# Optimization experiments

Measured on AMD Instinct MI355X. Metric: run time of the kernel, lower is better.

Reference implementation:

```python
import jax, jax.numpy as jnp
import numpy as np

NUM_NODES = 200000
NUM_EDGES = 500000
B = 4096            # batch size (src, dst, neg each B)
ND = 3 * B          # dst nodes of attention block
K = 10              # sampled neighbors per dst
N = ND * (1 + K)    # total tail nodes
D = 128             # dim_embed == dim_node
DE = 128            # dim_edge
DT = 128            # dim_time
H = 2               # num_heads
DIN = 2 * D + DE + DT  # GRUCell input dim


def time_encode(t, w, b):
    # tglite TimeEncode: cos(t * w + b)
    return jnp.cos(t[..., None] * w + b)


def gru_cell(x, h, w_ih, w_hh, b_ih, b_hh):
    # torch.nn.GRUCell, gate order [r, z, n]
    gi = x @ w_ih.T + b_ih
    gh = h @ w_hh.T + b_hh
    i_r, i_z, i_n = jnp.split(gi, 3, axis=-1)
    h_r, h_z, h_n = jnp.split(gh, 3, axis=-1)
    r = jax.nn.sigmoid(i_r + h_r)
    z = jax.nn.sigmoid(i_z + h_z)
    n = jnp.tanh(i_n + r * h_n)
    return (1.0 - z) * n + z * h


def setup_inputs() -> dict:
    key = jax.random.key(0)
    ks = jax.random.split(key, 40)
    p = lambda i, shape: jax.random.normal(ks[i], shape, dtype=jnp.float32) * 0.05
    return {
        "nodes": jax.random.randint(ks[0], (N,), 0, NUM_NODES),
        "eids": jax.random.randint(ks[1], (ND, K), 0, NUM_EDGES),
        "dt_nbr": jax.random.uniform(ks[2], (ND, K), dtype=jnp.float32) * 1000.0,
        "nfeat": p(3, (NUM_NODES, D)),
        "mem_data": p(4, (NUM_NODES, D)),
        "mem_time": jax.random.uniform(ks[5], (NUM_NODES,), dtype=jnp.float32) * 1000.0,
        "mail_data": p(6, (NUM_NODES, 2 * D + DE)),
        "mail_time": jax.random.uniform(ks[7], (NUM_NODES,), dtype=jnp.float32) * 1000.0,
        "efeat": p(8, (NUM_EDGES, DE)),
        "time_w": p(9, (DT,)),
        "time_b": p(10, (DT,)),
        "gru_w_ih": p(11, (3 * D, DIN)),
        "gru_w_hh": p(12, (3 * D, D)),
        "gru_b_ih": p(13, (3 * D,)),
        "gru_b_hh": p(14, (3 * D,)),
        "wq": p(15, (D, D + DT)), "bq": p(16, (D,)),
        "wk": p(17, (D, D + DE + DT)), "bk": p(18, (D,)),
        "wv": p(19, (D, D + DE + DT)), "bv": p(20, (D,)),
        "wo": p(21, (D, 2 * D)), "bo": p(22, (D,)),
        "ln_g": jnp.ones((D,), jnp.float32), "ln_b": jnp.zeros((D,), jnp.float32),
        "ep_sw": p(23, (D, D)), "ep_sb": p(24, (D,)),
        "ep_dw": p(25, (D, D)), "ep_db": p(26, (D,)),
        "ep_ow": p(27, (1, D)), "ep_ob": p(28, (1,)),
    }


def reference(nodes, eids, dt_nbr, nfeat, mem_data, mem_time, mail_data, mail_time,
              efeat, time_w, time_b, gru_w_ih, gru_w_hh, gru_b_ih, gru_b_hh,
              wq, bq, wk, bk, wv, bv, wo, bo, ln_g, ln_b,
              ep_sw, ep_sb, ep_dw, ep_db, ep_ow, ep_ob):
    # ---- update_memory: gather mailbox/memory, time-encode delta, GRUCell ----
    delta = mail_time[nodes] - mem_time[nodes]                  # [N]
    tenc = time_encode(delta, time_w, time_b)                   # [N, DT]
    mail = jnp.concatenate([mail_data[nodes], tenc], axis=1)    # [N, DIN]
    mem = gru_cell(mail, mem_data[nodes], gru_w_ih, gru_w_hh, gru_b_ih, gru_b_hh)  # [N, D]
    # (blk.g.mem.update(nodes, mem, mail_ts) is a persistent-state side effect)

    h = nfeat[nodes] + mem                                      # dst/src hidden states
    dst_h = h[:ND]                                              # [ND, D]
    src_h = h[ND:].reshape(ND, K, D)                            # [ND, K, D]

    # ---- TemporalAttnLayer (TGL-style multi-head attention over neighbors) ----
    zero_tenc = jnp.broadcast_to(jnp.cos(time_b), (ND, DT))     # time_encode(0)
    Q = jnp.concatenate([dst_h, zero_tenc], axis=1) @ wq.T + bq # [ND, D]
    tenc_n = time_encode(dt_nbr, time_w, time_b)                # [ND, K, DT]
    k_in = jnp.concatenate([src_h, efeat[eids], tenc_n], axis=-1)  # [ND, K, D+DE+DT]
    Kf = k_in @ wk.T + bk                                       # [ND, K, D]
    Vf = k_in @ wv.T + bv                                       # [ND, K, D]

    dh = D // H
    Qh = Q.reshape(ND, H, dh)
    Kh = Kf.reshape(ND, K, H, dh)
    Vh = Vf.reshape(ND, K, H, dh)
    att = jax.nn.softmax(jnp.einsum('nhd,nkhd->nkh', Qh, Kh), axis=1)  # [ND, K, H]
    agg = jnp.einsum('nkh,nkhd->nhd', att, Vh).reshape(ND, D)   # [ND, D]

    out = jnp.concatenate([dst_h, agg], axis=1) @ wo.T + bo     # [ND, D]
    out = jax.nn.relu(out)
    mu = out.mean(axis=-1, keepdims=True)
    var = out.var(axis=-1, keepdims=True)
    emb = ln_g * (out - mu) * jax.lax.rsqrt(var + 1e-5) + ln_b  # LayerNorm

    # ---- EdgePredictor over (src, dst) and (src, neg) splits ----
    src_e, dst_e, neg_e = emb[:B], emb[B:2 * B], emb[2 * B:]
    s_proj = src_e @ ep_sw.T + ep_sb
    pos = jax.nn.relu(s_proj + dst_e @ ep_dw.T + ep_db) @ ep_ow.T + ep_ob  # [B, 1]
    neg = jax.nn.relu(s_proj + neg_e @ ep_dw.T + ep_db) @ ep_ow.T + ep_ob  # [B, 1]
    return jnp.concatenate([pos, neg], axis=1)                  # [B, 2]
```

## Files before the change

kernel.cpp:

```cpp
#include <hip/hip_runtime.h>

constexpr int ND_   = 12288;
constexpr int K_    = 10;
constexpr int NTOT  = ND_ * (1 + K_);
constexpr int B_    = 4096;
constexpr int RKV   = ND_ * K_;

constexpr size_t OFF_QB   = 0;
constexpr size_t OFF_AGG  = 786432;
constexpr size_t OFF_HB   = 43253760;
constexpr size_t OFF_KVB  = 51904512;
constexpr size_t OFF_EMB  = 67633152;
constexpr size_t OFF_WCAT = 69206016;
constexpr size_t OFF_WKV  = 69369856;
constexpr size_t OFF_BCAT = 69419008;
constexpr size_t OFF_BKV  = 69419520;
constexpr size_t OFF_WQB  = 69419776;
constexpr size_t OFF_WOB  = 69427968;
constexpr size_t OFF_SWP  = 69444352;
constexpr size_t OFF_DWP  = 69460736;
constexpr size_t OFF_QZ   = 69477120;

#define DEVFN __device__ __forceinline__

typedef __attribute__((ext_vector_type(8))) short bf16x8;
typedef __attribute__((ext_vector_type(4))) float f32x4;
#define MFMA16(a, b, c) __builtin_amdgcn_mfma_f32_16x16x32_bf16((a), (b), (c), 0, 0, 0)

DEVFN unsigned short f2bf(float x) {
  unsigned int u = __float_as_uint(x);
  u = (u + 0x7FFFu + ((u >> 16) & 1u)) >> 16;
  return (unsigned short)u;
}
DEVFN float bf2f(unsigned short h) { return __uint_as_float(((unsigned int)h) << 16); }

DEVFN bf16x8 packcvt(float4 a, float4 b) {
  union { unsigned int u[4]; bf16x8 v; } r;
  asm("v_cvt_pk_bf16_f32 %0, %1, %2" : "=v"(r.u[0]) : "v"(a.x), "v"(a.y));
  asm("v_cvt_pk_bf16_f32 %0, %1, %2" : "=v"(r.u[1]) : "v"(a.z), "v"(a.w));
  asm("v_cvt_pk_bf16_f32 %0, %1, %2" : "=v"(r.u[2]) : "v"(b.x), "v"(b.y));
  asm("v_cvt_pk_bf16_f32 %0, %1, %2" : "=v"(r.u[3]) : "v"(b.z), "v"(b.w));
  return r.v;
}

DEVFN float dot4(const float4 a, const float4 b, float acc) {
  acc = fmaf(a.x, b.x, acc);
  acc = fmaf(a.y, b.y, acc);
  acc = fmaf(a.z, b.z, acc);
  acc = fmaf(a.w, b.w, acc);
  return acc;
}
DEVFN float sigmoidf_(float x) { return 1.0f / (1.0f + expf(-x)); }

__global__ void k0_all(const float* __restrict__ w_ih, const float* __restrict__ w_hh,
                       const float* __restrict__ wk,   const float* __restrict__ wv,
                       const float* __restrict__ wq,   const float* __restrict__ wo,
                       const float* __restrict__ sw,   const float* __restrict__ dwm,
                       const float* __restrict__ b_ih, const float* __restrict__ b_hh,
                       const float* __restrict__ bk,   const float* __restrict__ bv,
                       const float* __restrict__ time_b, const float* __restrict__ bq,
                       unsigned short* __restrict__ WcatP, unsigned short* __restrict__ WkvP,
                       unsigned short* __restrict__ WqB,   unsigned short* __restrict__ WoB,
                       float4* __restrict__ SwP, float4* __restrict__ DwP,
                       float* __restrict__ bcat, float* __restrict__ bkv,
                       float* __restrict__ qzero)
{
  int gid = blockIdx.x * 256 + threadIdx.x;
  if (gid < 327680) {
    int f = gid >> 9, idx = gid & 511;
    int l = idx >> 3, j8 = idx & 7;
    int kt = f >> 5, nt = f & 31;
    int k = kt * 32 + (l >> 4) * 8 + j8;
    int c = nt * 16 + (l & 15);
    int q = c >> 7, jb = (c >> 6) & 1, g = (c >> 4) & 3, j = q * 32 + jb * 16 + (c & 15);
    float w;
    if (g == 0)      w = (k < 512) ? w_ih[(size_t)j * 512 + k]         : w_hh[(size_t)j * 128 + (k - 512)];
    else if (g == 1) w = (k < 512) ? w_ih[(size_t)(128 + j) * 512 + k] : w_hh[(size_t)(128 + j) * 128 + (k - 512)];
    else if (g == 2) w = (k < 512) ? w_ih[(size_t)(256 + j) * 512 + k] : 0.0f;
    else             w = (k < 512) ? 0.0f : w_hh[(size_t)(256 + j) * 128 + (k - 512)];
    WcatP[gid] = f2bf(w);
    return;
  }
  gid -= 327680;
  if (gid < 98304) {
    int f = gid >> 9, idx = gid & 511;
    int l = idx >> 3, j8 = idx & 7;
    int kt = f >> 4, nt = f & 15;
    int k = kt * 32 + (l >> 4) * 8 + j8;
    int c = nt * 16 + (l & 15);
    float w = (c < 128) ? wk[(size_t)c * 384 + k] : wv[(size_t)(c - 128) * 384 + k];
    WkvP[gid] = f2bf(w);
    return;
  }
  gid -= 98304;
  if (gid < 49152) {
    if (gid < 16384) {
      int f = gid >> 9, idx = gid & 511;
      int l = idx >> 3, j8 = idx & 7;
      int kt = f >> 3, nt = f & 7;
      int k = kt * 32 + (l >> 4) * 8 + j8;
      int c = nt * 16 + (l & 15);
      WqB[gid] = f2bf(wq[(size_t)c * 256 + k]);
    } else {
      int g2 = gid - 16384;
      int f = g2 >> 9, idx = g2 & 511;
      int l = idx >> 3, j8 = idx & 7;
      int kt = f >> 3, nt = f & 7;
      int k = kt * 32 + (l >> 4) * 8 + j8;
      int c = nt * 16 + (l & 15);
      WoB[g2] = f2bf(wo[(size_t)c * 256 + k]);
    }
    return;
  }
  gid -= 49152;
  if (gid < 8960) {
    if (gid < 4096) {
      int k4 = gid / 128, c = gid % 128;
      const float* s = sw + c * 128 + 4 * k4;
      SwP[gid] = make_float4(s[0], s[1], s[2], s[3]);
    } else if (gid < 8192) {
      int id = gid - 4096;
      int k4 = id / 128, c = id % 128;
      const float* s = dwm + c * 128 + 4 * k4;
      DwP[id] = make_float4(s[0], s[1], s[2], s[3]);
    } else if (gid < 8704) {
      int id = gid - 8192;
      int q = id >> 7, jb = (id >> 6) & 1, g = (id >> 4) & 3, lcc = id & 15;
      int j = q * 32 + jb * 16 + lcc;
      float b;
      if (g == 0)      b = b_ih[j] + b_hh[j];
      else if (g == 1) b = b_ih[128 + j] + b_hh[128 + j];
      else if (g == 2) b = b_ih[256 + j];
      else             b = b_hh[256 + j];
      bcat[id] = b;
    } else {
      int id = gid - 8704;
      bkv[id] = (id < 128) ? bk[id] : bv[id - 128];
    }
    return;
  }
  gid -= 8960;
  if (gid < 128) {
    float acc = bq[gid];
    for (int k = 0; k < 128; ++k)
      acc = fmaf(cosf(time_b[k]), wq[gid * 256 + 128 + k], acc);
    qzero[gid] = acc;
  }
}

__global__ __launch_bounds__(512) void k1_fused(
    const int* __restrict__ nodes, const float* __restrict__ mail_data,
    const float* __restrict__ mem_data, const float* __restrict__ mail_time,
    const float* __restrict__ mem_time, const float* __restrict__ time_w,
    const float* __restrict__ time_b, const unsigned short* __restrict__ WcatP,
    const float* __restrict__ bcat, const float* __restrict__ nfeat,
    unsigned short* __restrict__ hb)
{
  __shared__ unsigned short As[20 * 1024];
  __shared__ int nid[32];
  __shared__ float dd[32];
  const int tid = threadIdx.x;
  const int rbase = blockIdx.x * 32;
  if (tid < 32) {
    int n = nodes[rbase + tid];
    nid[tid] = n;
    dd[tid] = mail_time[n] - mem_time[n];
  }
  __syncthreads();

  {
    const int sr = tid & 31, tcol = tid >> 5;
    const int sc4 = tcol & 7, koff = tcol >> 3;
    const int n = nid[sr];
    const float drow = dd[sr];
    const float* mailp = mail_data + (size_t)n * 384;
    const float* memp  = mem_data  + (size_t)n * 128;
    const int half = sr >> 4, r15 = sr & 15, q = sc4 >> 1;
    const int slot = half * 64 + q * 16 + ((r15 + 4 * q) & 15);
    char* wbase = (char*)As + slot * 16 + (sc4 & 1) * 8;
    #pragma unroll
    for (int i = 0; i < 10; ++i) {
      const int kt = 2 * i + koff;
      const int c0 = kt * 32 + sc4 * 4;
      float4 v;
      if (i < 6) {
        v = *(const float4*)(mailp + c0);
      } else if (i >= 8) {
        v = *(const float4*)(memp + c0 - 512);
      } else {
        const float4 w0 = *(const float4*)(time_w + (c0 - 384));
        const float4 b0 = *(const float4*)(time_b + (c0 - 384));
        v.x = cosf(fmaf(drow, w0.x, b0.x)); v.y = cosf(fmaf(drow, w0.y, b0.y));
        v.z = cosf(fmaf(drow, w0.z, b0.z)); v.w = cosf(fmaf(drow, w0.w, b0.w));
      }
      unsigned int pk0, pk1;
      asm("v_cvt_pk_bf16_f32 %0, %1, %2" : "=v"(pk0) : "v"(v.x), "v"(v.y));
      asm("v_cvt_pk_bf16_f32 %0, %1, %2" : "=v"(pk1) : "v"(v.z), "v"(v.w));
      *(uint2*)(wbase + kt * 2048) = make_uint2(pk0, pk1);
    }
  }
  __syncthreads();

  const int w = tid >> 6, l = tid & 63;
  const int lr = l >> 4, lc = l & 15;
  const unsigned short* Bp = WcatP + (size_t)(w * 4) * 512 + l * 8;
  const int slotA = lr * 16 + ((lc + 4 * lr) & 15);
  const char* rbA = (const char*)As + slotA * 16;

  f32x4 acc[2][4];
  #pragma unroll
  for (int m = 0; m < 2; ++m)
    #pragma unroll
    for (int bn = 0; bn < 4; ++bn) acc[m][bn] = (f32x4){0.f, 0.f, 0.f, 0.f};

  #pragma unroll
  for (int kt = 0; kt < 20; ++kt) {
    const bf16x8 A0 = *(const bf16x8*)(rbA + kt * 2048);
    const bf16x8 A1 = *(const bf16x8*)(rbA + kt * 2048 + 1024);
    #pragma unroll
    for (int bn = 0; bn < 4; ++bn) {
      const bf16x8 Bf = *(const bf16x8*)(Bp + ((size_t)kt * 32 + bn) * 512);
      acc[0][bn] = MFMA16(A0, Bf, acc[0][bn]);
      acc[1][bn] = MFMA16(A1, Bf, acc[1][bn]);
    }
  }

  const int jcol = (w >> 1) * 32 + (w & 1) * 16 + lc;
  float bg[4];
  #pragma unroll
  for (int g = 0; g < 4; ++g) bg[g] = bcat[w * 64 + g * 16 + lc];

  #pragma unroll
  for (int mt = 0; mt < 2; ++mt) {
    #pragma unroll
    for (int rr = 0; rr < 4; ++rr) {
      const int rloc = mt * 16 + lr * 4 + rr;
      const int grow = rbase + rloc;
      const int n2   = nid[rloc];
      const float aR  = acc[mt][0][rr] + bg[0];
      const float aZ  = acc[mt][1][rr] + bg[1];
      const float aNi = acc[mt][2][rr] + bg[2];
      const float aNh = acc[mt][3][rr] + bg[3];
      const float r_  = sigmoidf_(aR);
      const float z_  = sigmoidf_(aZ);
      const float n_  = tanhf(aNi + r_ * aNh);
      const float mem = mem_data[(size_t)n2 * 128 + jcol];
      const float h = nfeat[(size_t)n2 * 128 + jcol] + (1.0f - z_) * n_ + z_ * mem;
      hb[(size_t)grow * 128 + jcol] = f2bf(h);
    }
  }
}

DEVFN void k2s(const unsigned short* __restrict__ WkvP, int kt, int wn, int l,
               bf16x8 a, f32x4 (&acc)[4]) {
  #pragma unroll
  for (int bn = 0; bn < 4; ++bn) {
    const bf16x8 b = *(const bf16x8*)(WkvP + ((size_t)(kt * 16 + wn * 4 + bn) * 64 + l) * 8);
    acc[bn] = MFMA16(a, b, acc[bn]);
  }
}

__global__ __launch_bounds__(512) void k2_fused(
    const unsigned short* __restrict__ hb, const int* __restrict__ eids,
    const float* __restrict__ dt_nbr, const float* __restrict__ efeat,
    const float* __restrict__ time_w, const float* __restrict__ time_b,
    const unsigned short* __restrict__ WkvP, const float* __restrict__ bkv,
    unsigned short* __restrict__ KVb)
{
  const int w = threadIdx.x >> 6, l = threadIdx.x & 63;
  const int wm = w >> 2, wn = w & 3;
  const int lr = l >> 4, lc = l & 15;
  const int t16 = blockIdx.x * 2 + wm;
  const int rbase = t16 * 16;

  int eld = 0; float dld = 0.f;
  if (l < 16) { eld = eids[rbase + l]; dld = dt_nbr[rbase + l]; }
  const int   eid = __shfl(eld, lc);
  const float dt  = __shfl(dld, lc);

  const float* ep = efeat + (size_t)eid * 128 + lr * 8;
  bf16x8 ea[4];
  #pragma unroll
  for (int qq = 0; qq < 4; ++qq)
    ea[qq] = packcvt(((const float4*)(ep + qq * 32))[0], ((const float4*)(ep + qq * 32))[1]);
  const unsigned short* hp = hb + (size_t)(ND_ + rbase + lc) * 128 + lr * 8;
  bf16x8 hh[4];
  #pragma unroll
  for (int qq = 0; qq < 4; ++qq) hh[qq] = *(const bf16x8*)(hp + qq * 32);
  bf16x8 tt[4];
  #pragma unroll
  for (int qq = 0; qq < 4; ++qq) {
    const int c0 = qq * 32 + lr * 8;
    const float4 w0 = ((const float4*)(time_w + c0))[0];
    const float4 w1 = ((const float4*)(time_w + c0))[1];
    const float4 b0 = ((const float4*)(time_b + c0))[0];
    const float4 b1 = ((const float4*)(time_b + c0))[1];
    float4 u, v;
    u.x = cosf(fmaf(dt, w0.x, b0.x)); u.y = cosf(fmaf(dt, w0.y, b0.y));
    u.z = cosf(fmaf(dt, w0.z, b0.z)); u.w = cosf(fmaf(dt, w0.w, b0.w));
    v.x = cosf(fmaf(dt, w1.x, b1.x)); v.y = cosf(fmaf(dt, w1.y, b1.y));
    v.z = cosf(fmaf(dt, w1.z, b1.z)); v.w = cosf(fmaf(dt, w1.w, b1.w));
    tt[qq] = packcvt(u, v);
  }

  f32x4 acc[4];
  #pragma unroll
  for (int bn = 0; bn < 4; ++bn) acc[bn] = (f32x4){0.f, 0.f, 0.f, 0.f};

  #pragma unroll
  for (int qq = 0; qq < 4; ++qq) k2s(WkvP, qq, wn, l, hh[qq], acc);
  #pragma unroll
  for (int qq = 0; qq < 4; ++qq) k2s(WkvP, 4 + qq, wn, l, ea[qq], acc);
  #pragma unroll
  for (int qq = 0; qq < 4; ++qq) k2s(WkvP, 8 + qq, wn, l, tt[qq], acc);

  float bb[4];
  #pragma unroll
  for (int bn = 0; bn < 4; ++bn) bb[bn] = bkv[wn * 64 + bn * 16 + lc];

  #pragma unroll
  for (int rr = 0; rr < 4; ++rr) {
    const size_t grow = (size_t)(rbase + lr * 4 + rr);
    #pragma unroll
    for (int bn = 0; bn < 4; ++bn)
      KVb[grow * 256 + wn * 64 + bn * 16 + lc] = f2bf(acc[bn][rr] + bb[bn]);
  }
}

__global__ __launch_bounds__(512) void kQ_gemm(
    const unsigned short* __restrict__ hb, const unsigned short* __restrict__ WqB,
    const float* __restrict__ qzero, unsigned short* __restrict__ Qb)
{
  const int w = threadIdx.x >> 6, l = threadIdx.x & 63;
  const int wm = w >> 2, wn = w & 3;
  const int lr = l >> 4, lc = l & 15;
  const int t16base = blockIdx.x * 4 + wm * 2;
  const unsigned short* Ar0 = hb + (size_t)(t16base * 16 + lc) * 128 + lr * 8;
  const unsigned short* Ar1 = Ar0 + 16 * 128;

  f32x4 acc[2][2];
  #pragma unroll
  for (int m = 0; m < 2; ++m)
    #pragma unroll
    for (int bn = 0; bn < 2; ++bn) acc[m][bn] = (f32x4){0.f, 0.f, 0.f, 0.f};

  #pragma unroll
  for (int kt = 0; kt < 4; ++kt) {
    const bf16x8 a0 = *(const bf16x8*)(Ar0 + kt * 32);
    const bf16x8 a1 = *(const bf16x8*)(Ar1 + kt * 32);
    #pragma unroll
    for (int bn = 0; bn < 2; ++bn) {
      const bf16x8 b = *(const bf16x8*)(WqB + ((size_t)(kt * 8 + wn * 2 + bn) * 64 + l) * 8);
      acc[0][bn] = MFMA16(a0, b, acc[0][bn]);
      acc[1][bn] = MFMA16(a1, b, acc[1][bn]);
    }
  }

  #pragma unroll
  for (int mt = 0; mt < 2; ++mt)
    #pragma unroll
    for (int rr = 0; rr < 4; ++rr) {
      const int row = (t16base + mt) * 16 + lr * 4 + rr;
      #pragma unroll
      for (int bn = 0; bn < 2; ++bn) {
        const int col = (wn * 2 + bn) * 16 + lc;
        Qb[(size_t)row * 128 + col] = f2bf(acc[mt][bn][rr] + qzero[col]);
      }
    }
}

__global__ __launch_bounds__(256) void kAtt(
    const unsigned short* __restrict__ Qb, const unsigned short* __restrict__ KVb,
    unsigned short* __restrict__ aggb)
{
  const int w = threadIdx.x >> 6, l = threadIdx.x & 63;
  const int i = blockIdx.x * 4 + w;
  const float q0 = bf2f(Qb[(size_t)i * 128 + l]);
  const float q1 = bf2f(Qb[(size_t)i * 128 + 64 + l]);
  const unsigned short* base = KVb + (size_t)i * K_ * 256;

  float s0[K_], s1[K_], v0[K_], v1[K_];
  #pragma unroll
  for (int kk = 0; kk < K_; ++kk) {
    const unsigned short* rp = base + kk * 256;
    const float k0 = bf2f(rp[l]);
    const float k1 = bf2f(rp[64 + l]);
    v0[kk] = bf2f(rp[128 + l]);
    v1[kk] = bf2f(rp[192 + l]);
    float p0 = q0 * k0, p1 = q1 * k1;
    #pragma unroll
    for (int t = 32; t; t >>= 1) { p0 += __shfl_xor(p0, t); p1 += __shfl_xor(p1, t); }
    s0[kk] = p0; s1[kk] = p1;
  }
  float m0 = s0[0], m1 = s1[0];
  #pragma unroll
  for (int kk = 1; kk < K_; ++kk) { m0 = fmaxf(m0, s0[kk]); m1 = fmaxf(m1, s1[kk]); }
  float sum0 = 0.f, sum1 = 0.f, a0 = 0.f, a1 = 0.f;
  #pragma unroll
  for (int kk = 0; kk < K_; ++kk) {
    const float e0 = expf(s0[kk] - m0);
    const float e1 = expf(s1[kk] - m1);
    sum0 += e0; sum1 += e1;
    a0 += e0 * v0[kk]; a1 += e1 * v1[kk];
  }
  aggb[(size_t)i * 128 + l]      = f2bf(a0 / sum0);
  aggb[(size_t)i * 128 + 64 + l] = f2bf(a1 / sum1);
}

__global__ __launch_bounds__(512) void kO_ln(
    const unsigned short* __restrict__ hb, const unsigned short* __restrict__ aggb,
    const unsigned short* __restrict__ WoB, const float* __restrict__ bo,
    const float* __restrict__ ln_g, const float* __restrict__ ln_b,
    float* __restrict__ emb)
{
  __shared__ float ps[64][4], pq[64][4];
  const int w = threadIdx.x >> 6, l = threadIdx.x & 63;
  const int wm = w >> 2, wn = w & 3;
  const int lr = l >> 4, lc = l & 15;
  const int t16base = blockIdx.x * 4 + wm * 2;
  const unsigned short* Ah0 = hb   + (size_t)(t16base * 16 + lc) * 128 + lr * 8;
  const unsigned short* Ah1 = Ah0 + 16 * 128;
  const unsigned short* Ag0 = aggb + (size_t)(t16base * 16 + lc) * 128 + lr * 8;
  const unsigned short* Ag1 = Ag0 + 16 * 128;

  f32x4 acc[2][2];
  #pragma unroll
  for (int m = 0; m < 2; ++m)
    #pragma unroll
    for (int bn = 0; bn < 2; ++bn) acc[m][bn] = (f32x4){0.f, 0.f, 0.f, 0.f};

  #pragma unroll
  for (int kt = 0; kt < 8; ++kt) {
    const bf16x8 a0 = (kt < 4) ? *(const bf16x8*)(Ah0 + kt * 32)
                               : *(const bf16x8*)(Ag0 + (kt - 4) * 32);
    const bf16x8 a1 = (kt < 4) ? *(const bf16x8*)(Ah1 + kt * 32)
                               : *(const bf16x8*)(Ag1 + (kt - 4) * 32);
    #pragma unroll
    for (int bn = 0; bn < 2; ++bn) {
      const bf16x8 b = *(const bf16x8*)(WoB + ((size_t)(kt * 8 + wn * 2 + bn) * 64 + l) * 8);
      acc[0][bn] = MFMA16(a0, b, acc[0][bn]);
      acc[1][bn] = MFMA16(a1, b, acc[1][bn]);
    }
  }

  const int c0 = (wn * 2) * 16 + lc, c1 = c0 + 16;
  const float b0v = bo[c0], b1v = bo[c1];
  float xv0[2][4], xv1[2][4];
  #pragma unroll
  for (int mt = 0; mt < 2; ++mt)
    #pragma unroll
    for (int rr = 0; rr < 4; ++rr) {
      const float x0 = fmaxf(acc[mt][0][rr] + b0v, 0.f);
      const float x1 = fmaxf(acc[mt][1][rr] + b1v, 0.f);
      xv0[mt][rr] = x0; xv1[mt][rr] = x1;
      float s = x0 + x1, q = x0 * x0 + x1 * x1;
      #pragma unroll
      for (int t = 8; t; t >>= 1) { s += __shfl_xor(s, t); q += __shfl_xor(q, t); }
      const int rloc = (wm * 2 + mt) * 16 + lr * 4 + rr;
      if (lc == 0) { ps[rloc][wn] = s; pq[rloc][wn] = q; }
    }
  __syncthreads();
  const float g0 = ln_g[c0], g1 = ln_g[c1], lb0 = ln_b[c0], lb1 = ln_b[c1];
  #pragma unroll
  for (int mt = 0; mt < 2; ++mt)
    #pragma unroll
    for (int rr = 0; rr < 4; ++rr) {
      const int rloc = (wm * 2 + mt) * 16 + lr * 4 + rr;
      const int row  = blockIdx.x * 64 + rloc;
      const float sum = ps[rloc][0] + ps[rloc][1] + ps[rloc][2] + ps[rloc][3];
      const float sq  = pq[rloc][0] + pq[rloc][1] + pq[rloc][2] + pq[rloc][3];
      const float mu  = sum * (1.0f / 128.0f);
      const float var = sq * (1.0f / 128.0f) - mu * mu;
      const float rs  = rsqrtf(var + 1e-5f);
      emb[(size_t)row * 128 + c0] = g0 * (xv0[mt][rr] - mu) * rs + lb0;
      emb[(size_t)row * 128 + c1] = g1 * (xv1[mt][rr] - mu) * rs + lb1;
    }
}

__global__ __launch_bounds__(128) void k3_ep(
    const float* __restrict__ emb, const float4* __restrict__ SwP,
    const float4* __restrict__ DwP, const float* __restrict__ ep_sb,
    const float* __restrict__ ep_db, const float* __restrict__ ep_ow,
    const float* __restrict__ ep_ob, float* __restrict__ out)
{
  __shared__ float se[128], de[128], ne[128];
  __shared__ float redp[2], redn[2];
  const int c = threadIdx.x;
  const int i = blockIdx.x;
  se[c] = emb[(size_t)i * 128 + c];
  de[c] = emb[(size_t)(B_ + i) * 128 + c];
  ne[c] = emb[(size_t)(2 * B_ + i) * 128 + c];
  __syncthreads();
  float sacc = ep_sb[c], dacc = ep_db[c], nacc = ep_db[c];
  for (int k4 = 0; k4 < 32; ++k4) {
    const float4 sw = SwP[k4 * 128 + c];
    const float4 dw = DwP[k4 * 128 + c];
    sacc = dot4(((const float4*)se)[k4], sw, sacc);
    dacc = dot4(((const float4*)de)[k4], dw, dacc);
    nacc = dot4(((const float4*)ne)[k4], dw, nacc);
  }
  const float ow = ep_ow[c];
  float pp = fmaxf(sacc + dacc, 0.f) * ow;
  float pn = fmaxf(sacc + nacc, 0.f) * ow;
  for (int t = 32; t; t >>= 1) { pp += __shfl_xor(pp, t); pn += __shfl_xor(pn, t); }
  if ((c & 63) == 0) { redp[c >> 6] = pp; redn[c >> 6] = pn; }
  __syncthreads();
  if (c == 0) {
    const float ob = ep_ob[0];
    out[i * 2]     = redp[0] + redp[1] + ob;
    out[i * 2 + 1] = redn[0] + redn[1] + ob;
  }
}

extern "C" void kernel_launch(void* const* d_in, const int* in_sizes, int n_in,
                              void* d_out, int out_size, void* d_ws, size_t ws_size,
                              hipStream_t stream) {
  const int*   nodes     = (const int*)d_in[0];
  const int*   eids      = (const int*)d_in[1];
  const float* dt_nbr    = (const float*)d_in[2];
  const float* nfeat     = (const float*)d_in[3];
  const float* mem_data  = (const float*)d_in[4];
  const float* mem_time  = (const float*)d_in[5];
  const float* mail_data = (const float*)d_in[6];
  const float* mail_time = (const float*)d_in[7];
  const float* efeat     = (const float*)d_in[8];
  const float* time_w    = (const float*)d_in[9];
  const float* time_b    = (const float*)d_in[10];
  const float* gru_w_ih  = (const float*)d_in[11];
  const float* gru_w_hh  = (const float*)d_in[12];
  const float* gru_b_ih  = (const float*)d_in[13];
  const float* gru_b_hh  = (const float*)d_in[14];
  const float* wq        = (const float*)d_in[15];
  const float* bq        = (const float*)d_in[16];
  const float* wk        = (const float*)d_in[17];
  const float* bk        = (const float*)d_in[18];
  const float* wv        = (const float*)d_in[19];
  const float* bv        = (const float*)d_in[20];
  const float* wo        = (const float*)d_in[21];
  const float* bo        = (const float*)d_in[22];
  const float* ln_g      = (const float*)d_in[23];
  const float* ln_b      = (const float*)d_in[24];
  const float* ep_sw     = (const float*)d_in[25];
  const float* ep_sb     = (const float*)d_in[26];
  const float* ep_dw     = (const float*)d_in[27];
  const float* ep_db     = (const float*)d_in[28];
  const float* ep_ow     = (const float*)d_in[29];
  const float* ep_ob     = (const float*)d_in[30];
  float* out = (float*)d_out;
  float* ws  = (float*)d_ws;

  unsigned short* Qb    = (unsigned short*)(ws + OFF_QB);
  unsigned short* aggb  = (unsigned short*)(ws + OFF_AGG);
  unsigned short* hb    = (unsigned short*)(ws + OFF_HB);
  unsigned short* KVb   = (unsigned short*)(ws + OFF_KVB);
  float*          emb   = ws + OFF_EMB;
  unsigned short* WcatP = (unsigned short*)(ws + OFF_WCAT);
  unsigned short* WkvP  = (unsigned short*)(ws + OFF_WKV);
  float*          bcat  = ws + OFF_BCAT;
  float*          bkv   = ws + OFF_BKV;
  unsigned short* WqB   = (unsigned short*)(ws + OFF_WQB);
  unsigned short* WoB   = (unsigned short*)(ws + OFF_WOB);
  float4*         SwP   = (float4*)(ws + OFF_SWP);
  float4*         DwP   = (float4*)(ws + OFF_DWP);
  float*          qzero = ws + OFF_QZ;

  k0_all<<<1892, 256, 0, stream>>>(gru_w_ih, gru_w_hh, wk, wv, wq, wo, ep_sw, ep_dw,
                                   gru_b_ih, gru_b_hh, bk, bv, time_b, bq,
                                   WcatP, WkvP, WqB, WoB, SwP, DwP, bcat, bkv, qzero);
  k1_fused<<<NTOT / 32, 512, 0, stream>>>(nodes, mail_data, mem_data, mail_time,
                                          mem_time, time_w, time_b, WcatP, bcat,
                                          nfeat, hb);
  k2_fused<<<RKV / 32, 512, 0, stream>>>(hb, eids, dt_nbr, efeat, time_w, time_b,
                                         WkvP, bkv, KVb);
  kQ_gemm<<<ND_ / 64, 512, 0, stream>>>(hb, WqB, qzero, Qb);
  kAtt<<<ND_ / 4, 256, 0, stream>>>(Qb, KVb, aggb);
  kO_ln<<<ND_ / 64, 512, 0, stream>>>(hb, aggb, WoB, bo, ln_g, ln_b, emb);
  k3_ep<<<B_, 128, 0, stream>>>(emb, SwP, DwP, ep_sb, ep_db, ep_ow, ep_ob, out);
}
```

Before: 406.5 us.

## Retile GRU kernel to 64-row blocks and switch to fast intrinsic math

The fused memory-update GRU kernel now processes 64 rows per block instead of 32. Each wave computes a 32x128 output tile, so each weight fragment loaded from global memory is reused across twice as many rows. The shared-memory staging layout and gather are rewritten to match, and the launch bounds ask for higher occupancy. Separately, cosf, expf, tanhf and division in the GRU, time-encoding and attention code are replaced with fast intrinsics (__cosf, __expf, __fdividef, an exp-based tanh). This lowers transcendental cost at some loss of accuracy, for example __cosf on time arguments that can reach about 1000*w.

```diff
diff --git a/kernel.cpp b/kernel.cpp
--- a/kernel.cpp
+++ b/kernel.cpp
@@ -50,7 +50,12 @@
   acc = fmaf(a.w, b.w, acc);
   return acc;
 }
-DEVFN float sigmoidf_(float x) { return 1.0f / (1.0f + expf(-x)); }
+DEVFN float fsig(float x)  { return __fdividef(1.0f, 1.0f + __expf(-x)); }
+DEVFN float ftanh(float x) {
+  x = fminf(fmaxf(x, -15.0f), 15.0f);
+  const float t = __expf(2.0f * x);
+  return __fdividef(t - 1.0f, t + 1.0f);
+}
 
 __global__ void k0_all(const float* __restrict__ w_ih, const float* __restrict__ w_hh,
                        const float* __restrict__ wk,   const float* __restrict__ wv,
@@ -148,7 +153,7 @@
   }
 }
 
-__global__ __launch_bounds__(512) void k1_fused(
+__global__ __launch_bounds__(512, 4) void k1_fused(
     const int* __restrict__ nodes, const float* __restrict__ mail_data,
     const float* __restrict__ mem_data, const float* __restrict__ mail_time,
     const float* __restrict__ mem_time, const float* __restrict__ time_w,
@@ -156,97 +161,93 @@
     const float* __restrict__ bcat, const float* __restrict__ nfeat,
     unsigned short* __restrict__ hb)
 {
-  __shared__ unsigned short As[20 * 1024];
-  __shared__ int nid[32];
-  __shared__ float dd[32];
+  __shared__ unsigned short As[20 * 2048];
   const int tid = threadIdx.x;
-  const int rbase = blockIdx.x * 32;
-  if (tid < 32) {
-    int n = nodes[rbase + tid];
-    nid[tid] = n;
-    dd[tid] = mail_time[n] - mem_time[n];
-  }
-  __syncthreads();
+  const int rbase = blockIdx.x * 64;
 
   {
-    const int sr = tid & 31, tcol = tid >> 5;
-    const int sc4 = tcol & 7, koff = tcol >> 3;
-    const int n = nid[sr];
-    const float drow = dd[sr];
+    const int sr = tid & 63, scol = tid >> 6;
+    const int koff = scol >> 2, q = scol & 3;
+    const int n = nodes[rbase + sr];
+    const float drow = mail_time[n] - mem_time[n];
     const float* mailp = mail_data + (size_t)n * 384;
     const float* memp  = mem_data  + (size_t)n * 128;
-    const int half = sr >> 4, r15 = sr & 15, q = sc4 >> 1;
-    const int slot = half * 64 + q * 16 + ((r15 + 4 * q) & 15);
-    char* wbase = (char*)As + slot * 16 + (sc4 & 1) * 8;
+    unsigned short* wb = As + ((size_t)((sr >> 4) * 64 + q * 16 + (sr & 15))) * 8;
     #pragma unroll
     for (int i = 0; i < 10; ++i) {
       const int kt = 2 * i + koff;
-      const int c0 = kt * 32 + sc4 * 4;
-      float4 v;
-      if (i < 6) {
-        v = *(const float4*)(mailp + c0);
-      } else if (i >= 8) {
-        v = *(const float4*)(memp + c0 - 512);
+      const int c0 = kt * 32 + q * 8;
+      float4 v0, v1;
+      if (c0 < 384) {
+        v0 = *(const float4*)(mailp + c0);
+        v1 = *(const float4*)(mailp + c0 + 4);
+      } else if (c0 >= 512) {
+        v0 = *(const float4*)(memp + c0 - 512);
+        v1 = *(const float4*)(memp + c0 - 508);
       } else {
-        const float4 w0 = *(const float4*)(time_w + (c0 - 384));
-        const float4 b0 = *(const float4*)(time_b + (c0 - 384));
-        v.x = cosf(fmaf(drow, w0.x, b0.x)); v.y = cosf(fmaf(drow, w0.y, b0.y));
-        v.z = cosf(fmaf(drow, w0.z, b0.z)); v.w = cosf(fmaf(drow, w0.w, b0.w));
+        const float4 w0 = *(const float4*)(time_w + c0 - 384);
+        const float4 w1 = *(const float4*)(time_w + c0 - 380);
+        const float4 b0 = *(const float4*)(time_b + c0 - 384);
+        const float4 b1 = *(const float4*)(time_b + c0 - 380);
+        v0.x = __cosf(fmaf(drow, w0.x, b0.x)); v0.y = __cosf(fmaf(drow, w0.y, b0.y));
+        v0.z = __cosf(fmaf(drow, w0.z, b0.z)); v0.w = __cosf(fmaf(drow, w0.w, b0.w));
+        v1.x = __cosf(fmaf(drow, w1.x, b1.x)); v1.y = __cosf(fmaf(drow, w1.y, b1.y));
+        v1.z = __cosf(fmaf(drow, w1.z, b1.z)); v1.w = __cosf(fmaf(drow, w1.w, b1.w));
       }
-      unsigned int pk0, pk1;
-      asm("v_cvt_pk_bf16_f32 %0, %1, %2" : "=v"(pk0) : "v"(v.x), "v"(v.y));
-      asm("v_cvt_pk_bf16_f32 %0, %1, %2" : "=v"(pk1) : "v"(v.z), "v"(v.w));
-      *(uint2*)(wbase + kt * 2048) = make_uint2(pk0, pk1);
+      *(bf16x8*)(wb + (size_t)kt * 2048) = packcvt(v0, v1);
     }
   }
   __syncthreads();
 
   const int w = tid >> 6, l = tid & 63;
+  const int wm = w >> 2, wn = w & 3;
   const int lr = l >> 4, lc = l & 15;
-  const unsigned short* Bp = WcatP + (size_t)(w * 4) * 512 + l * 8;
-  const int slotA = lr * 16 + ((lc + 4 * lr) & 15);
-  const char* rbA = (const char*)As + slotA * 16;
-
-  f32x4 acc[2][4];
+  const unsigned short* Bp = WcatP + (size_t)(wn * 8) * 512 + l * 8;
+  const unsigned short* Ab = As + (size_t)(2 * wm) * 512 + (size_t)l * 8;
+
+  f32x4 acc[2][8];
   #pragma unroll
   for (int m = 0; m < 2; ++m)
     #pragma unroll
-    for (int bn = 0; bn < 4; ++bn) acc[m][bn] = (f32x4){0.f, 0.f, 0.f, 0.f};
+    for (int bn = 0; bn < 8; ++bn) acc[m][bn] = (f32x4){0.f, 0.f, 0.f, 0.f};
 
   #pragma unroll
   for (int kt = 0; kt < 20; ++kt) {
-    const bf16x8 A0 = *(const bf16x8*)(rbA + kt * 2048);
-    const bf16x8 A1 = *(const bf16x8*)(rbA + kt * 2048 + 1024);
-    #pragma unroll
-    for (int bn = 0; bn < 4; ++bn) {
+    const bf16x8 A0 = *(const bf16x8*)(Ab + (size_t)kt * 2048);
+    const bf16x8 A1 = *(const bf16x8*)(Ab + (size_t)kt * 2048 + 512);
+    #pragma unroll
+    for (int bn = 0; bn < 8; ++bn) {
       const bf16x8 Bf = *(const bf16x8*)(Bp + ((size_t)kt * 32 + bn) * 512);
       acc[0][bn] = MFMA16(A0, Bf, acc[0][bn]);
       acc[1][bn] = MFMA16(A1, Bf, acc[1][bn]);
     }
   }
 
-  const int jcol = (w >> 1) * 32 + (w & 1) * 16 + lc;
-  float bg[4];
-  #pragma unroll
-  for (int g = 0; g < 4; ++g) bg[g] = bcat[w * 64 + g * 16 + lc];
+  float bg[8];
+  #pragma unroll
+  for (int bn = 0; bn < 8; ++bn) bg[bn] = bcat[wn * 128 + bn * 16 + lc];
 
   #pragma unroll
   for (int mt = 0; mt < 2; ++mt) {
     #pragma unroll
     for (int rr = 0; rr < 4; ++rr) {
-      const int rloc = mt * 16 + lr * 4 + rr;
+      const int rloc = (2 * wm + mt) * 16 + lr * 4 + rr;
       const int grow = rbase + rloc;
-      const int n2   = nid[rloc];
-      const float aR  = acc[mt][0][rr] + bg[0];
-      const float aZ  = acc[mt][1][rr] + bg[1];
-      const float aNi = acc[mt][2][rr] + bg[2];
-      const float aNh = acc[mt][3][rr] + bg[3];
-      const float r_  = sigmoidf_(aR);
-      const float z_  = sigmoidf_(aZ);
-      const float n_  = tanhf(aNi + r_ * aNh);
-      const float mem = mem_data[(size_t)n2 * 128 + jcol];
-      const float h = nfeat[(size_t)n2 * 128 + jcol] + (1.0f - z_) * n_ + z_ * mem;
-      hb[(size_t)grow * 128 + jcol] = f2bf(h);
+      const int n2   = nodes[grow];
+      #pragma unroll
+      for (int jb = 0; jb < 2; ++jb) {
+        const int jcol = wn * 32 + jb * 16 + lc;
+        const float aR  = acc[mt][jb * 4 + 0][rr] + bg[jb * 4 + 0];
+        const float aZ  = acc[mt][jb * 4 + 1][rr] + bg[jb * 4 + 1];
+        const float aNi = acc[mt][jb * 4 + 2][rr] + bg[jb * 4 + 2];
+        const float aNh = acc[mt][jb * 4 + 3][rr] + bg[jb * 4 + 3];
+        const float r_  = fsig(aR);
+        const float z_  = fsig(aZ);
+        const float n_  = ftanh(aNi + r_ * aNh);
+        const float mem = mem_data[(size_t)n2 * 128 + jcol];
+        const float h = nfeat[(size_t)n2 * 128 + jcol] + (1.0f - z_) * n_ + z_ * mem;
+        hb[(size_t)grow * 128 + jcol] = f2bf(h);
+      }
     }
   }
 }
@@ -296,10 +297,10 @@
     const float4 b0 = ((const float4*)(time_b + c0))[0];
     const float4 b1 = ((const float4*)(time_b + c0))[1];
     float4 u, v;
-    u.x = cosf(fmaf(dt, w0.x, b0.x)); u.y = cosf(fmaf(dt, w0.y, b0.y));
-    u.z = cosf(fmaf(dt, w0.z, b0.z)); u.w = cosf(fmaf(dt, w0.w, b0.w));
-    v.x = cosf(fmaf(dt, w1.x, b1.x)); v.y = cosf(fmaf(dt, w1.y, b1.y));
-    v.z = cosf(fmaf(dt, w1.z, b1.z)); v.w = cosf(fmaf(dt, w1.w, b1.w));
+    u.x = __cosf(fmaf(dt, w0.x, b0.x)); u.y = __cosf(fmaf(dt, w0.y, b0.y));
+    u.z = __cosf(fmaf(dt, w0.z, b0.z)); u.w = __cosf(fmaf(dt, w0.w, b0.w));
+    v.x = __cosf(fmaf(dt, w1.x, b1.x)); v.y = __cosf(fmaf(dt, w1.y, b1.y));
+    v.z = __cosf(fmaf(dt, w1.z, b1.z)); v.w = __cosf(fmaf(dt, w1.w, b1.w));
     tt[qq] = packcvt(u, v);
   }
 
@@ -398,13 +399,13 @@
   float sum0 = 0.f, sum1 = 0.f, a0 = 0.f, a1 = 0.f;
   #pragma unroll
   for (int kk = 0; kk < K_; ++kk) {
-    const float e0 = expf(s0[kk] - m0);
-    const float e1 = expf(s1[kk] - m1);
+    const float e0 = __expf(s0[kk] - m0);
+    const float e1 = __expf(s1[kk] - m1);
     sum0 += e0; sum1 += e1;
     a0 += e0 * v0[kk]; a1 += e1 * v1[kk];
   }
-  aggb[(size_t)i * 128 + l]      = f2bf(a0 / sum0);
-  aggb[(size_t)i * 128 + 64 + l] = f2bf(a1 / sum1);
+  aggb[(size_t)i * 128 + l]      = f2bf(__fdividef(a0, sum0));
+  aggb[(size_t)i * 128 + 64 + l] = f2bf(__fdividef(a1, sum1));
 }
 
 __global__ __launch_bounds__(512) void kO_ln(
@@ -567,7 +568,7 @@
   k0_all<<<1892, 256, 0, stream>>>(gru_w_ih, gru_w_hh, wk, wv, wq, wo, ep_sw, ep_dw,
                                    gru_b_ih, gru_b_hh, bk, bv, time_b, bq,
                                    WcatP, WkvP, WqB, WoB, SwP, DwP, bcat, bkv, qzero);
-  k1_fused<<<NTOT / 32, 512, 0, stream>>>(nodes, mail_data, mem_data, mail_time,
+  k1_fused<<<NTOT / 64, 512, 0, stream>>>(nodes, mail_data, mem_data, mail_time,
                                           mem_time, time_w, time_b, WcatP, bcat,
                                           nfeat, hb);
   k2_fused<<<RKV / 32, 512, 0, stream>>>(hb, eids, dt_nbr, efeat, time_w, time_b,
```

After: 546.3 us. +34.4%, slower.
